# Kernel optimization log

Measured on AMD Instinct MI355X. Metric: run time of the kernel, lower is better.

The kernel has to match this reference:

```python
import jax, jax.numpy as jnp
import numpy as np
import math

# Model dims (from init_kwargs + mamba_ssm Mamba2 defaults)
D_MODEL = 1024
EXPAND = 2
HEADDIM = 64
D_STATE = 64
D_CONV = 4
NGROUPS = 1
D_INNER = EXPAND * D_MODEL            # 2048
NHEADS = D_INNER // HEADDIM           # 32
CONV_DIM = D_INNER + 2 * NGROUPS * D_STATE   # 2176
D_IN_PROJ = 2 * D_INNER + 2 * NGROUPS * D_STATE + NHEADS  # 4256
BATCH, SEQLEN = 4, 2048
RMS_EPS = 1.1920929e-07   # torch.finfo(float32).eps (nn.RMSNorm eps=None)
GNORM_EPS = 1e-5          # mamba_ssm RMSNormGated eps


def _rmsnorm(x, w, eps):
    return x * jax.lax.rsqrt(jnp.mean(x * x, axis=-1, keepdims=True) + eps) * w


def setup_inputs() -> dict:
    key = jax.random.key(0)
    ks = jax.random.split(key, 8)
    x = jax.random.normal(ks[0], (BATCH, SEQLEN, D_MODEL), jnp.float32)
    # router MLP (Linear(d_model,32) -> SiLU -> Linear(32,3))
    r_w1 = jax.random.normal(ks[1], (32, D_MODEL), jnp.float32) / math.sqrt(D_MODEL)
    r_b1 = jnp.zeros((32,), jnp.float32)
    r_w2 = jax.random.normal(ks[2], (3, 32), jnp.float32) / math.sqrt(32)
    r_b2 = jnp.zeros((3,), jnp.float32)
    # Mamba2 params
    in_proj_w = jax.random.normal(ks[3], (D_IN_PROJ, D_MODEL), jnp.float32) / math.sqrt(D_MODEL)
    conv_w = jax.random.normal(ks[4], (CONV_DIM, D_CONV), jnp.float32) * 0.2
    conv_b = jnp.zeros((CONV_DIM,), jnp.float32)
    dt_bias = jax.random.normal(ks[5], (NHEADS,), jnp.float32) * 0.1
    # OrthoSSM multi-scale override: A_log[i] = log(0.001 * 2**i)
    A_log = jnp.log(0.001 * (2.0 ** jnp.arange(NHEADS, dtype=jnp.float32)))
    D_param = jnp.ones((NHEADS,), jnp.float32)
    gnorm_w = jnp.ones((D_INNER,), jnp.float32)
    out_proj_w = jax.random.normal(ks[6], (D_MODEL, D_INNER), jnp.float32) / math.sqrt(D_INNER)
    norm_w = jnp.ones((D_MODEL,), jnp.float32)
    return {"x": x, "norm_w": norm_w, "r_w1": r_w1, "r_b1": r_b1, "r_w2": r_w2,
            "r_b2": r_b2, "in_proj_w": in_proj_w, "conv_w": conv_w, "conv_b": conv_b,
            "dt_bias": dt_bias, "A_log": A_log, "D_param": D_param,
            "gnorm_w": gnorm_w, "out_proj_w": out_proj_w}


def _forward(x, norm_w, r_w1, r_b1, r_w2, r_b2, in_proj_w, conv_w, conv_b,
             dt_bias, A_log, D_param, gnorm_w, out_proj_w):
    B, S, Dm = x.shape
    x_norm = _rmsnorm(x, norm_w, RMS_EPS)
    # --- router: mean-pool -> tiny MLP -> softmax over 3 tiers ---
    h = jax.nn.silu(x_norm.mean(axis=1) @ r_w1.T + r_b1)
    probs = jax.nn.softmax(h @ r_w2.T + r_b2, axis=-1)   # [B,3]
    p_fast = probs[:, 0][:, None, None]
    p_mamba = (probs[:, 1] + probs[:, 2])[:, None, None]
    # --- Mamba2(x_norm) ---
    zxbcdt = x_norm @ in_proj_w.T                         # [B,S,4256]
    z, xBC, dt = jnp.split(zxbcdt, [D_INNER, D_INNER + CONV_DIM], axis=-1)
    # causal depthwise conv1d (kernel 4) + SiLU
    conv = jax.lax.conv_general_dilated(
        xBC.transpose(0, 2, 1), conv_w[:, None, :], (1,), [(D_CONV - 1, 0)],
        feature_group_count=CONV_DIM)                      # [B,CONV_DIM,S]
    xBC = jax.nn.silu(conv.transpose(0, 2, 1) + conv_b)    # [B,S,CONV_DIM]
    xh, Bmat, Cmat = jnp.split(xBC, [D_INNER, D_INNER + NGROUPS * D_STATE], axis=-1)
    xh = xh.reshape(B, S, NHEADS, HEADDIM)                 # [B,S,H,P]
    dt = jax.nn.softplus(dt + dt_bias)                     # [B,S,H]
    A = -jnp.exp(A_log)                                    # [H]
    dA = jnp.exp(dt * A)                                   # [B,S,H]

    def step(hstate, inp):
        dA_t, dt_t, x_t, B_t, C_t = inp
        # hstate: [B,H,P,N]
        hstate = hstate * dA_t[..., None, None] \
                 + (dt_t[..., None] * x_t)[..., None] * B_t[:, None, None, :]
        y_t = jnp.einsum('bhpn,bn->bhp', hstate, C_t)
        return hstate, y_t

    h0 = jnp.zeros((B, NHEADS, HEADDIM, D_STATE), x.dtype)
    xs = (dA.transpose(1, 0, 2), dt.transpose(1, 0, 2), xh.transpose(1, 0, 2, 3),
          Bmat.transpose(1, 0, 2), Cmat.transpose(1, 0, 2))
    _, ys = jax.lax.scan(step, h0, xs)                     # [S,B,H,P]
    y = ys.transpose(1, 0, 2, 3) + D_param[:, None] * xh   # D skip connection
    y = y.reshape(B, S, D_INNER)
    # gated RMSNorm: norm(y * silu(z)) * weight
    yg = y * jax.nn.silu(z)
    yg = _rmsnorm(yg, gnorm_w, GNORM_EPS)
    mamba_out = yg @ out_proj_w.T                          # [B,S,D]
    out = p_fast * x_norm + p_mamba * mamba_out
    return x + out


def reference(x, norm_w, r_w1, r_b1, r_w2, r_b2, in_proj_w, conv_w, conv_b,
              dt_bias, A_log, D_param, gnorm_w, out_proj_w):
    return _forward(x, norm_w, r_w1, r_b1, r_w2, r_b2, in_proj_w, conv_w, conv_b,
                    dt_bias, A_log, D_param, gnorm_w, out_proj_w)
```

## Files before the change

kernel.cpp:

```cpp
#include <hip/hip_runtime.h>
#include <math.h>

typedef __bf16 bf16;
typedef __bf16 bf16x8 __attribute__((ext_vector_type(8)));
typedef __bf16 bf16x4 __attribute__((ext_vector_type(4)));
typedef float f32x4 __attribute__((ext_vector_type(4)));

#define DEV static __device__ __forceinline__
#define AS1 __attribute__((address_space(1)))
#define AS3 __attribute__((address_space(3)))

constexpr int kBatch = 4, kSeq = 2048, kDModel = 1024;
constexpr int kDInner = 2048, kHeads = 32;
constexpr int kConvDim = 2176, kDInProj = 4256, kNPad1 = 4352;
constexpr int kRows = kBatch * kSeq;
constexpr int kChunk = 64, kNChunk = kSeq / kChunk;
constexpr float kRmsEps = 1.1920929e-07f;
constexpr float kGnEps = 1e-5f;
constexpr int kW1Blocks = kNPad1 * kDModel / 256;
constexpr int kW2Blocks = kDModel * kDInner / 1024;

DEV float siluf(float x) { return x / (1.f + expf(-x)); }

DEV float block_reduce_sum(float v, float* red, int tid) {
#pragma unroll
  for (int m = 1; m < 64; m <<= 1) v += __shfl_xor(v, m);
  if ((tid & 63) == 0) red[tid >> 6] = v;
  __syncthreads();
  return red[0] + red[1] + red[2] + red[3];
}

__global__ __launch_bounds__(256) void k_pre(
    const float* __restrict__ x, const float* __restrict__ nw,
    bf16* __restrict__ xnb, float* __restrict__ rs,
    const float* __restrict__ w1, bf16* __restrict__ w1b,
    const float* __restrict__ w2, const float* __restrict__ gw,
    bf16* __restrict__ w2b) {
  const int blk = blockIdx.x;
  const int tid = threadIdx.x;
  if (blk < kRows) {
    const int row = blk;
    float4 v = ((const float4*)(x + (size_t)row * kDModel))[tid];
    __shared__ float red[4];
    float ss = block_reduce_sum(v.x * v.x + v.y * v.y + v.z * v.z + v.w * v.w, red, tid);
    float scale = rsqrtf(ss * (1.f / kDModel) + kRmsEps);
    if (tid == 0) rs[row] = scale;
    float4 wv = ((const float4*)nw)[tid];
    bf16x4 ov;
    ov[0] = (bf16)(v.x * scale * wv.x);
    ov[1] = (bf16)(v.y * scale * wv.y);
    ov[2] = (bf16)(v.z * scale * wv.z);
    ov[3] = (bf16)(v.w * scale * wv.w);
    *(bf16x4*)(xnb + (size_t)row * kDModel + tid * 4) = ov;
  } else if (blk < kRows + kW1Blocks) {
    const size_t idx = (size_t)(blk - kRows) * 256 + tid;
    const int row = (int)(idx >> 10);
    w1b[idx] = (bf16)(row < kDInProj ? w1[idx] : 0.f);
  } else {
    const size_t i4 = (size_t)(blk - kRows - kW1Blocks) * 256 + tid;
    const int k4 = (int)((i4 * 4) & (kDInner - 1));
    float4 v = ((const float4*)w2)[i4];
    float4 g = *(const float4*)(gw + k4);
    bf16x4 o;
    o[0] = (bf16)(v.x * g.x); o[1] = (bf16)(v.y * g.y);
    o[2] = (bf16)(v.z * g.z); o[3] = (bf16)(v.w * g.w);
    ((bf16x4*)w2b)[i4] = o;
  }
}

__global__ __launch_bounds__(128) void k_pool1(const bf16* __restrict__ xnb,
                                               float* __restrict__ part) {
  const int g = blockIdx.x, b = blockIdx.y;
  const int tid = threadIdx.x;
  const bf16* base = xnb + ((size_t)b * kSeq + (size_t)g * 32) * kDModel + tid * 8;
  float acc[8] = {0, 0, 0, 0, 0, 0, 0, 0};
  for (int r = 0; r < 32; ++r) {
    bf16x8 v = *(const bf16x8*)(base + (size_t)r * kDModel);
#pragma unroll
    for (int j = 0; j < 8; ++j) acc[j] += (float)v[j];
  }
  float* o = part + ((size_t)b * 64 + g) * kDModel + tid * 8;
#pragma unroll
  for (int j = 0; j < 8; ++j) o[j] = acc[j];
}

__global__ __launch_bounds__(256) void k_pool2(const float* __restrict__ part,
                                               float* __restrict__ mean) {
  const int idx = blockIdx.x * 256 + threadIdx.x;
  const int b = idx >> 10, d = idx & 1023;
  float s = 0.f;
  for (int g = 0; g < 64; ++g) s += part[((size_t)b * 64 + g) * kDModel + d];
  mean[idx] = s * (1.f / kSeq);
}

__global__ __launch_bounds__(128) void k_router(const float* __restrict__ mean,
                                                const float* __restrict__ w1,
                                                const float* __restrict__ b1,
                                                const float* __restrict__ w2,
                                                const float* __restrict__ b2,
                                                float* __restrict__ pfm) {
  __shared__ float hbuf[4][32];
  __shared__ float logit[4][3];
  const int t = threadIdx.x;
  {
    int b = t >> 5, j = t & 31;
    float s = b1[j];
    for (int d = 0; d < kDModel; ++d) s += mean[b * kDModel + d] * w1[j * kDModel + d];
    hbuf[b][j] = siluf(s);
  }
  __syncthreads();
  if (t < 12) {
    int b = t / 3, k = t % 3;
    float s = b2[k];
    for (int j = 0; j < 32; ++j) s += hbuf[b][j] * w2[k * 32 + j];
    logit[b][k] = s;
  }
  __syncthreads();
  if (t < 4) {
    float m = fmaxf(logit[t][0], fmaxf(logit[t][1], logit[t][2]));
    float e0 = expf(logit[t][0] - m), e1 = expf(logit[t][1] - m), e2 = expf(logit[t][2] - m);
    float inv = 1.f / (e0 + e1 + e2);
    pfm[t] = e0 * inv;
    pfm[4 + t] = (e1 + e2) * inv;
  }
}

template <int WM, int WN, int NF, bool FUSE>
DEV void gemm_body(bf16* lds, float* rs2s,
                   const bf16* __restrict__ A, const bf16* __restrict__ B,
                   bf16* __restrict__ Cb, const float* __restrict__ xres,
                   const float* __restrict__ rs, const float* __restrict__ nw,
                   const float* __restrict__ pfm, float* __restrict__ outf,
                   int K, int Nreal, int ldc, int ntn) {
  constexpr int THREADS = WM * WN * 64;
  constexpr int BM = WM * 64;
  constexpr int BN = WN * NF * 16;
  constexpr int NA = (BM * 4) / THREADS;
  constexpr int NB = (BN * 4) / THREADS;
  constexpr int VMN = NA + NB;
  constexpr int ASZ = (BM / 2) * 64;
  constexpr int BSZ = (BN / 2) * 64;
  const int tid = threadIdx.x;
  const int lane = tid & 63, wid = tid >> 6;
  const int wr = wid / WN, wc = wid % WN;
  const int lr = lane & 15, kb = lane >> 4;
  const int cpx = (int)gridDim.x >> 3;
  const int bid = ((int)blockIdx.x & 7) * cpx + ((int)blockIdx.x >> 3);
  const long n0 = (long)(bid % ntn) * BN;
  const long m0 = (long)(bid / ntn) * BM;

  f32x4 acc[4][NF];
#pragma unroll
  for (int i = 0; i < 4; ++i)
#pragma unroll
    for (int j = 0; j < NF; ++j) acc[i][j] = (f32x4){0.f, 0.f, 0.f, 0.f};
  float ssq[4] = {0.f, 0.f, 0.f, 0.f};

  const int nkt = K >> 5;

#define STAGE(pp, kt)                                                          \
  {                                                                            \
    const long koff = (long)(kt)*32;                                           \
    _Pragma("unroll") for (int j = 0; j < NA; ++j) {                           \
      int idx = j * THREADS + tid;                                             \
      int line = idx >> 3, sp = (idx & 7) ^ (line & 7);                        \
      int row = line * 2 + (sp >> 2), ch = sp & 3;                             \
      __builtin_amdgcn_global_load_lds(                                        \
          (const AS1 void*)(A + (m0 + row) * K + koff + ch * 8),               \
          (AS3 void*)((char*)(lds + (pp)*ASZ) + idx * 16), 16, 0, 0);          \
    }                                                                          \
    _Pragma("unroll") for (int j = 0; j < NB; ++j) {                           \
      int idx = j * THREADS + tid;                                             \
      int line = idx >> 3, sp = (idx & 7) ^ (line & 7);                        \
      int row = line * 2 + (sp >> 2), ch = sp & 3;                             \
      __builtin_amdgcn_global_load_lds(                                        \
          (const AS1 void*)(B + (n0 + row) * K + koff + ch * 8),               \
          (AS3 void*)((char*)(lds + 3 * ASZ + (pp)*BSZ) + idx * 16), 16, 0, 0);\
    }                                                                          \
  }
#define LOFF(r) (((r) >> 1) * 128 + (((((r)&1) << 2) | kb) ^ (((r) >> 1) & 7)) * 16)
#define RDA(pp, r) (*(const bf16x8*)((const char*)(lds + (pp)*ASZ) + LOFF(r)))
#define RDB(pp, r) (*(const bf16x8*)((const char*)(lds + 3 * ASZ + (pp)*BSZ) + LOFF(r)))

  STAGE(0, 0);
  STAGE(1, 1);

  int cur = 0;
  for (int t = 0; t < nkt; ++t) {
    if (t + 2 < nkt) {
      int sb = cur + 2; if (sb >= 3) sb -= 3;
      STAGE(sb, t + 2);
      if constexpr (VMN == 3) asm volatile("s_waitcnt vmcnt(6)" ::: "memory");
      else asm volatile("s_waitcnt vmcnt(8)" ::: "memory");
    } else if (t + 1 < nkt) {
      if constexpr (VMN == 3) asm volatile("s_waitcnt vmcnt(3)" ::: "memory");
      else asm volatile("s_waitcnt vmcnt(4)" ::: "memory");
    } else {
      asm volatile("s_waitcnt vmcnt(0)" ::: "memory");
    }
    __builtin_amdgcn_s_barrier();

    bf16x8 bv[NF], af0, af1, af2, af3;
#pragma unroll
    for (int nf = 0; nf < NF; ++nf) bv[nf] = RDB(cur, wc * (NF * 16) + nf * 16 + lr);
    af0 = RDA(cur, wr * 64 + lr);
    __builtin_amdgcn_sched_barrier(0);
    af1 = RDA(cur, wr * 64 + 16 + lr);
    __builtin_amdgcn_sched_barrier(0);
    asm volatile("s_waitcnt lgkmcnt(1)" ::: "memory");
    __builtin_amdgcn_sched_barrier(0);
    __builtin_amdgcn_s_setprio(1);
#pragma unroll
    for (int nf = 0; nf < NF; ++nf)
      acc[0][nf] = __builtin_amdgcn_mfma_f32_16x16x32_bf16(af0, bv[nf], acc[0][nf], 0, 0, 0);
    af2 = RDA(cur, wr * 64 + 32 + lr);
    af3 = RDA(cur, wr * 64 + 48 + lr);
    __builtin_amdgcn_sched_barrier(0);
    asm volatile("s_waitcnt lgkmcnt(2)" ::: "memory");
    __builtin_amdgcn_sched_barrier(0);
#pragma unroll
    for (int nf = 0; nf < NF; ++nf)
      acc[1][nf] = __builtin_amdgcn_mfma_f32_16x16x32_bf16(af1, bv[nf], acc[1][nf], 0, 0, 0);
    asm volatile("s_waitcnt lgkmcnt(0)" ::: "memory");
    __builtin_amdgcn_sched_barrier(0);
    __builtin_amdgcn_s_barrier();
#pragma unroll
    for (int nf = 0; nf < NF; ++nf)
      acc[2][nf] = __builtin_amdgcn_mfma_f32_16x16x32_bf16(af2, bv[nf], acc[2][nf], 0, 0, 0);
#pragma unroll
    for (int nf = 0; nf < NF; ++nf)
      acc[3][nf] = __builtin_amdgcn_mfma_f32_16x16x32_bf16(af3, bv[nf], acc[3][nf], 0, 0, 0);
    __builtin_amdgcn_s_setprio(0);

    if constexpr (FUSE) {
      if (wc == 0) {
#pragma unroll
        for (int e = 0; e < 8; ++e) {
          float f0 = (float)af0[e], f1 = (float)af1[e];
          float f2 = (float)af2[e], f3 = (float)af3[e];
          ssq[0] = fmaf(f0, f0, ssq[0]);
          ssq[1] = fmaf(f1, f1, ssq[1]);
          ssq[2] = fmaf(f2, f2, ssq[2]);
          ssq[3] = fmaf(f3, f3, ssq[3]);
        }
      }
    }
    cur = cur + 1 == 3 ? 0 : cur + 1;
  }
#undef STAGE
#undef LOFF
#undef RDA
#undef RDB

  const int rr = kb * 4;
  if constexpr (FUSE) {
    if (wc == 0) {
#pragma unroll
      for (int mf = 0; mf < 4; ++mf) {
        float v = ssq[mf];
        v += __shfl_xor(v, 16);
        v += __shfl_xor(v, 32);
        if (kb == 0) rs2s[wr * 64 + mf * 16 + lr] = rsqrtf(v * (1.f / kDInner) + kGnEps);
      }
    }
    __syncthreads();
    const int bx = (int)(m0 >> 11);
    const float pf = pfm[bx], pm = pfm[4 + bx];
#pragma unroll
    for (int mf = 0; mf < 4; ++mf) {
      long rbase = m0 + wr * 64 + mf * 16 + rr;
      float rsv[4], r2v[4];
#pragma unroll
      for (int j = 0; j < 4; ++j) {
        rsv[j] = rs[rbase + j];
        r2v[j] = rs2s[wr * 64 + mf * 16 + rr + j];
      }
#pragma unroll
      for (int nf = 0; nf < NF; ++nf) {
        int col = (int)n0 + wc * (NF * 16) + nf * 16 + lr;
        float wv = nw[col];
#pragma unroll
        for (int j = 0; j < 4; ++j) {
          size_t oi = (size_t)(rbase + j) * kDModel + col;
          float xv = xres[oi];
          outf[oi] = xv + pf * xv * rsv[j] * wv + pm * r2v[j] * acc[mf][nf][j];
        }
      }
    }
  } else {
    __syncthreads();
    bf16* scr = lds + wid * (16 * 72);
    const int srow = lane >> 2, cg = lane & 3;
#pragma unroll
    for (int mf = 0; mf < 4; ++mf) {
#pragma unroll
      for (int nf = 0; nf < NF; ++nf)
#pragma unroll
        for (int j = 0; j < 4; ++j)
          scr[(rr + j) * 72 + nf * 16 + lr] = (bf16)acc[mf][nf][j];
      asm volatile("s_waitcnt lgkmcnt(0)" ::: "memory");
      __builtin_amdgcn_sched_barrier(0);
      int col = (int)n0 + wc * (NF * 16) + cg * 16;
      if (col < Nreal) {
        long grow = m0 + wr * 64 + mf * 16 + srow;
        bf16x8 v0 = *(const bf16x8*)(scr + srow * 72 + cg * 16);
        bf16x8 v1 = *(const bf16x8*)(scr + srow * 72 + cg * 16 + 8);
        *(bf16x8*)(Cb + grow * (long)ldc + col) = v0;
        *(bf16x8*)(Cb + grow * (long)ldc + col + 8) = v1;
      }
      __builtin_amdgcn_sched_barrier(0);
    }
  }
}

__global__ __launch_bounds__(512, 4) void k_gemm_in(
    const bf16* __restrict__ A, const bf16* __restrict__ B,
    bf16* __restrict__ Cb, int K, int Nreal, int ldc, int ntn) {
  constexpr int ASZ = (128 / 2) * 64, BSZ = (256 / 2) * 64;
  __shared__ __align__(16) bf16 lds[3 * ASZ + 3 * BSZ];
  __shared__ float rs2s[128];
  gemm_body<2, 4, 4, false>(lds, rs2s, A, B, Cb, nullptr, nullptr, nullptr,
                            nullptr, nullptr, K, Nreal, ldc, ntn);
}

__global__ __launch_bounds__(256, 4) void k_gemm_out(
    const bf16* __restrict__ A, const bf16* __restrict__ B,
    const float* __restrict__ xres, const float* __restrict__ rs,
    const float* __restrict__ nw, const float* __restrict__ pfm,
    float* __restrict__ outf, int K, int Nreal, int ldc, int ntn) {
  constexpr int ASZ = (64 / 2) * 64, BSZ = (128 / 2) * 64;
  __shared__ __align__(16) bf16 lds[3 * ASZ + 3 * BSZ];
  __shared__ float rs2s[64];
  gemm_body<1, 4, 2, true>(lds, rs2s, A, B, nullptr, xres, rs, nw, pfm, outf,
                           K, Nreal, ldc, ntn);
}

__global__ __launch_bounds__(256) void k_convdt(const bf16* __restrict__ zx,
                                                const float* __restrict__ cw,
                                                const float* __restrict__ cb,
                                                bf16* __restrict__ xbc,
                                                const float* __restrict__ dt_bias,
                                                const float* __restrict__ A_log,
                                                float* __restrict__ dt,
                                                float* __restrict__ ldA) {
  const int gid = blockIdx.x * 256 + threadIdx.x;
  if (gid < kRows * 272) {
    const int row = gid / 272;
    const int cg = gid - row * 272;
    const int c0 = cg * 8;
    const int s = row & (kSeq - 1);
    const bf16* base = zx + (size_t)row * kDInProj + kDInner + c0;
    bf16x8 z8 = {};
    bf16x8 r3 = *(const bf16x8*)(base);
    bf16x8 r2 = (s >= 1) ? *(const bf16x8*)(base - kDInProj) : z8;
    bf16x8 r1 = (s >= 2) ? *(const bf16x8*)(base - 2 * kDInProj) : z8;
    bf16x8 r0 = (s >= 3) ? *(const bf16x8*)(base - 3 * kDInProj) : z8;
    bf16x8 o;
#pragma unroll
    for (int e = 0; e < 8; ++e) {
      float4 w = ((const float4*)cw)[c0 + e];
      float a = cb[c0 + e] + w.x * (float)r0[e] + w.y * (float)r1[e] +
                w.z * (float)r2[e] + w.w * (float)r3[e];
      o[e] = (bf16)siluf(a);
    }
    *(bf16x8*)(xbc + (size_t)row * kConvDim + c0) = o;
  } else {
    const int g2 = gid - kRows * 272;
    const int row = g2 >> 2, grp = g2 & 3;
    bf16x8 r8 = *(const bf16x8*)(zx + (size_t)row * kDInProj + (kDInner + kConvDim) + grp * 8);
#pragma unroll
    for (int e = 0; e < 8; ++e) {
      int hh = grp * 8 + e;
      float raw = (float)r8[e] + dt_bias[hh];
      float dtv = (raw > 20.f) ? raw : log1pf(expf(raw));
      dt[row * kHeads + hh] = dtv;
      ldA[row * kHeads + hh] = dtv * -expf(A_log[hh]);
    }
  }
}

__global__ __launch_bounds__(256) void k_chunkA(
    const bf16* __restrict__ xbc, const float* __restrict__ dtb,
    const float* __restrict__ ldab, float* __restrict__ cumbuf,
    float* __restrict__ Tc, bf16* __restrict__ yb, bf16* __restrict__ Sbuf) {
  const int c = blockIdx.x, h = blockIdx.y, b = blockIdx.z;
  const int tid = threadIdx.x;
  const int w = tid >> 6, lane = tid & 63, lr = lane & 15, kb = lane >> 4;
  const int rr = kb * 4;
  const int t0 = c * kChunk;
  __shared__ bf16 Bl[64 * 72], Cl[64 * 72], XT[64 * 72], WBT[64 * 72], Ml[64 * 72];
  __shared__ float cum_s[64], dt_s[64], w_s[64];

  {
    int s = tid >> 2, q = tid & 3;
    const bf16* rowp = xbc + ((size_t)b * kSeq + t0 + s) * kConvDim;
    bf16x8 x0 = *(const bf16x8*)(rowp + h * 64 + q * 16);
    bf16x8 x1 = *(const bf16x8*)(rowp + h * 64 + q * 16 + 8);
    bf16x8 b0 = *(const bf16x8*)(rowp + kDInner + q * 16);
    bf16x8 b1 = *(const bf16x8*)(rowp + kDInner + q * 16 + 8);
    bf16x8 c0 = *(const bf16x8*)(rowp + kDInner + 64 + q * 16);
    bf16x8 c1 = *(const bf16x8*)(rowp + kDInner + 64 + q * 16 + 8);
    *(bf16x8*)(Bl + s * 72 + q * 16) = b0;
    *(bf16x8*)(Bl + s * 72 + q * 16 + 8) = b1;
    *(bf16x8*)(Cl + s * 72 + q * 16) = c0;
    *(bf16x8*)(Cl + s * 72 + q * 16 + 8) = c1;
#pragma unroll
    for (int e = 0; e < 8; ++e) XT[(q * 16 + e) * 72 + s] = x0[e];
#pragma unroll
    for (int e = 0; e < 8; ++e) XT[(q * 16 + 8 + e) * 72 + s] = x1[e];
  }
  if (tid < 64) {
    size_t di = ((size_t)b * kSeq + t0 + tid) * kHeads + h;
    float v = ldab[di];
    float dtv = dtb[di];
#pragma unroll
    for (int o = 1; o < 64; o <<= 1) {
      float u = __shfl_up(v, o);
      if (lane >= o) v += u;
    }
    cum_s[tid] = v;
    dt_s[tid] = dtv;
    float tot = __shfl(v, 63);
    w_s[tid] = expf(tot - v) * dtv;
    cumbuf[(((size_t)b * kHeads + h) * kNChunk + c) * 64 + tid] = v;
    if (tid == 63) Tc[(b * kHeads + h) * kNChunk + c] = expf(v);
  }
  __syncthreads();

#pragma unroll
  for (int i = 0; i < 16; ++i) {
    int e = i * 256 + tid;
    int n = e >> 6, s = e & 63;
    WBT[n * 72 + s] = (bf16)((float)Bl[s * 72 + n] * w_s[s]);
  }

  f32x4 g[4];
#pragma unroll
  for (int nt = 0; nt < 4; ++nt) g[nt] = (f32x4){0.f, 0.f, 0.f, 0.f};
#pragma unroll
  for (int kk = 0; kk < 2; ++kk) {
    bf16x8 a = *(const bf16x8*)(Cl + (w * 16 + lr) * 72 + kk * 32 + kb * 8);
#pragma unroll
    for (int nt = 0; nt < 4; ++nt) {
      bf16x8 bb = *(const bf16x8*)(Bl + (nt * 16 + lr) * 72 + kk * 32 + kb * 8);
      g[nt] = __builtin_amdgcn_mfma_f32_16x16x32_bf16(a, bb, g[nt], 0, 0, 0);
    }
  }
#pragma unroll
  for (int nt = 0; nt < 4; ++nt)
#pragma unroll
    for (int j = 0; j < 4; ++j) {
      int tt = w * 16 + rr + j, ss = nt * 16 + lr;
      float m = (ss <= tt) ? g[nt][j] * expf(cum_s[tt] - cum_s[ss]) * dt_s[ss] : 0.f;
      Ml[tt * 72 + ss] = (bf16)m;
    }
  __syncthreads();

  f32x4 y4[4];
#pragma unroll
  for (int pt = 0; pt < 4; ++pt) y4[pt] = (f32x4){0.f, 0.f, 0.f, 0.f};
#pragma unroll
  for (int kk = 0; kk < 2; ++kk) {
    bf16x8 a = *(const bf16x8*)(Ml + (w * 16 + lr) * 72 + kk * 32 + kb * 8);
#pragma unroll
    for (int pt = 0; pt < 4; ++pt) {
      bf16x8 bb = *(const bf16x8*)(XT + (pt * 16 + lr) * 72 + kk * 32 + kb * 8);
      y4[pt] = __builtin_amdgcn_mfma_f32_16x16x32_bf16(a, bb, y4[pt], 0, 0, 0);
    }
  }
  f32x4 s4[4];
#pragma unroll
  for (int nt = 0; nt < 4; ++nt) s4[nt] = (f32x4){0.f, 0.f, 0.f, 0.f};
#pragma unroll
  for (int kk = 0; kk < 2; ++kk) {
    bf16x8 a = *(const bf16x8*)(XT + (w * 16 + lr) * 72 + kk * 32 + kb * 8);
#pragma unroll
    for (int nt = 0; nt < 4; ++nt) {
      bf16x8 bb = *(const bf16x8*)(WBT + (nt * 16 + lr) * 72 + kk * 32 + kb * 8);
      s4[nt] = __builtin_amdgcn_mfma_f32_16x16x32_bf16(a, bb, s4[nt], 0, 0, 0);
    }
  }
#pragma unroll
  for (int pt = 0; pt < 4; ++pt)
#pragma unroll
    for (int j = 0; j < 4; ++j) {
      Bl[(w * 16 + rr + j) * 72 + pt * 16 + lr] = (bf16)y4[pt][j];
      Cl[(w * 16 + rr + j) * 72 + pt * 16 + lr] = (bf16)s4[pt][j];
    }
  __syncthreads();
  {
    int row = tid >> 2, cg = tid & 3;
    bf16x8 v0 = *(const bf16x8*)(Bl + row * 72 + cg * 16);
    bf16x8 v1 = *(const bf16x8*)(Bl + row * 72 + cg * 16 + 8);
    bf16* dst = yb + ((size_t)b * kSeq + t0 + row) * kDInner + h * 64 + cg * 16;
    *(bf16x8*)dst = v0;
    *(bf16x8*)(dst + 8) = v1;
    const size_t sbase = (((size_t)b * kHeads + h) * kNChunk + c) * 4096;
    bf16x8 u0 = *(const bf16x8*)(Cl + row * 72 + cg * 16);
    bf16x8 u1 = *(const bf16x8*)(Cl + row * 72 + cg * 16 + 8);
    bf16* sdst = Sbuf + sbase + row * 64 + cg * 16;
    *(bf16x8*)sdst = u0;
    *(bf16x8*)(sdst + 8) = u1;
  }
}

__global__ __launch_bounds__(256) void k_chunkB(bf16* __restrict__ S,
                                                const float* __restrict__ Tc) {
  const int gid = blockIdx.x * 256 + threadIdx.x;
  const int bh = gid >> 10;
  const int pn = (gid & 1023) << 2;
  bf16* base = S + (size_t)bh * kNChunk * 4096 + pn;
  const float* tc = Tc + bh * kNChunk;
  float4 hh = {0.f, 0.f, 0.f, 0.f};
  bf16x4 s = *(const bf16x4*)(base);
  for (int c = 0; c < kNChunk; ++c) {
    bf16x4 sn = {};
    if (c + 1 < kNChunk) sn = *(const bf16x4*)(base + (size_t)(c + 1) * 4096);
    float t = tc[c];
    bf16x4 ho;
    ho[0] = (bf16)hh.x; ho[1] = (bf16)hh.y; ho[2] = (bf16)hh.z; ho[3] = (bf16)hh.w;
    *(bf16x4*)(base + (size_t)c * 4096) = ho;
    hh.x = t * hh.x + (float)s[0];
    hh.y = t * hh.y + (float)s[1];
    hh.z = t * hh.z + (float)s[2];
    hh.w = t * hh.w + (float)s[3];
    s = sn;
  }
}

__global__ __launch_bounds__(256) void k_chunkC(
    const bf16* __restrict__ xbc, const bf16* __restrict__ zx,
    const float* __restrict__ cumbuf, const bf16* __restrict__ hs,
    const float* __restrict__ Dp, bf16* __restrict__ yb) {
  const int c = blockIdx.x, h = blockIdx.y, b = blockIdx.z;
  const int tid = threadIdx.x;
  const int w = tid >> 6, lane = tid & 63, lr = lane & 15, kb = lane >> 4;
  const int rr = kb * 4;
  const int t0 = c * kChunk;
  __shared__ bf16 Cl[64 * 72];
  __shared__ float ecum[64];
  __shared__ float scrf[64 * 68];
  {
    int s = tid >> 2, q = tid & 3;
    const bf16* rowp = xbc + ((size_t)b * kSeq + t0 + s) * kConvDim + kDInner + 64 + q * 16;
    *(bf16x8*)(Cl + s * 72 + q * 16) = *(const bf16x8*)rowp;
    *(bf16x8*)(Cl + s * 72 + q * 16 + 8) = *(const bf16x8*)(rowp + 8);
  }
  if (tid < 64)
    ecum[tid] = expf(cumbuf[(((size_t)b * kHeads + h) * kNChunk + c) * 64 + tid]);
  __syncthreads();

  const bf16* hbase = hs + (((size_t)b * kHeads + h) * kNChunk + c) * 4096;
  f32x4 acc[4];
#pragma unroll
  for (int pt = 0; pt < 4; ++pt) acc[pt] = (f32x4){0.f, 0.f, 0.f, 0.f};
#pragma unroll
  for (int kk = 0; kk < 2; ++kk) {
    bf16x8 a = *(const bf16x8*)(Cl + (w * 16 + lr) * 72 + kk * 32 + kb * 8);
#pragma unroll
    for (int pt = 0; pt < 4; ++pt) {
      bf16x8 bb = *(const bf16x8*)(hbase + (pt * 16 + lr) * 64 + kk * 32 + kb * 8);
      acc[pt] = __builtin_amdgcn_mfma_f32_16x16x32_bf16(a, bb, acc[pt], 0, 0, 0);
    }
  }
#pragma unroll
  for (int pt = 0; pt < 4; ++pt)
#pragma unroll
    for (int j = 0; j < 4; ++j) {
      int tt = w * 16 + rr + j;
      scrf[tt * 68 + pt * 16 + lr] = ecum[tt] * acc[pt][j];
    }
  __syncthreads();
  {
    const float Dh = Dp[h];
    int row = tid >> 2, cg = tid & 3;
    size_t ri = (size_t)b * kSeq + t0 + row;
    const float* sp = scrf + row * 68 + cg * 16;
    bf16* yp = yb + ri * kDInner + h * 64 + cg * 16;
    const bf16* xp = xbc + ri * kConvDim + h * 64 + cg * 16;
    const bf16* zp = zx + ri * kDInProj + h * 64 + cg * 16;
#pragma unroll
    for (int half = 0; half < 2; ++half) {
      bf16x8 yv = *(const bf16x8*)(yp + half * 8);
      bf16x8 xv = *(const bf16x8*)(xp + half * 8);
      bf16x8 zv = *(const bf16x8*)(zp + half * 8);
      bf16x8 o;
#pragma unroll
      for (int e = 0; e < 8; ++e) {
        float yfull = (float)yv[e] + sp[half * 8 + e] + Dh * (float)xv[e];
        o[e] = (bf16)(yfull * siluf((float)zv[e]));
      }
      *(bf16x8*)(yp + half * 8) = o;
    }
  }
}

extern "C" void kernel_launch(void* const* d_in, const int* in_sizes, int n_in,
                              void* d_out, int out_size, void* d_ws, size_t ws_size,
                              hipStream_t stream) {
  const float* x = (const float*)d_in[0];
  const float* norm_w = (const float*)d_in[1];
  const float* r_w1 = (const float*)d_in[2];
  const float* r_b1 = (const float*)d_in[3];
  const float* r_w2 = (const float*)d_in[4];
  const float* r_b2 = (const float*)d_in[5];
  const float* in_proj_w = (const float*)d_in[6];
  const float* conv_w = (const float*)d_in[7];
  const float* conv_b = (const float*)d_in[8];
  const float* dt_bias = (const float*)d_in[9];
  const float* A_log = (const float*)d_in[10];
  const float* D_param = (const float*)d_in[11];
  const float* gnorm_w = (const float*)d_in[12];
  const float* out_proj_w = (const float*)d_in[13];
  float* out = (float*)d_out;
  char* ws = (char*)d_ws;

  bf16* xnb     = (bf16*)(ws + 0);
  bf16* w1b     = (bf16*)(ws + 16777216);
  bf16* zx      = (bf16*)(ws + 25690112);
  bf16* xbc     = (bf16*)(ws + 95420416);
  float* dtb    = (float*)(ws + 131072000);
  float* ldab   = (float*)(ws + 132120576);
  float* cumbuf = (float*)(ws + 133169152);
  float* Tcb    = (float*)(ws + 134217728);
  bf16* yb      = (bf16*)(ws + 134234112);
  bf16* Sbuf    = (bf16*)(ws + 167788544);
  bf16* w2b     = (bf16*)(ws + 201342976);
  float* part   = (float*)(ws + 205537280);
  float* meanb  = (float*)(ws + 206585856);
  float* pfm    = (float*)(ws + 206602240);
  float* rsb    = (float*)(ws + 206602368);

  k_pre<<<kRows + kW1Blocks + kW2Blocks, 256, 0, stream>>>(
      x, norm_w, xnb, rsb, in_proj_w, w1b, out_proj_w, gnorm_w, w2b);
  k_pool1<<<dim3(64, 4), 128, 0, stream>>>(xnb, part);
  k_pool2<<<16, 256, 0, stream>>>(part, meanb);
  k_router<<<1, 128, 0, stream>>>(meanb, r_w1, r_b1, r_w2, r_b2, pfm);
  k_gemm_in<<<(kRows / 128) * (kNPad1 / 256), 512, 0, stream>>>(
      xnb, w1b, zx, kDModel, kDInProj, kDInProj, kNPad1 / 256);
  k_convdt<<<(kRows * 272 + kRows * 4) / 256, 256, 0, stream>>>(
      zx, conv_w, conv_b, xbc, dt_bias, A_log, dtb, ldab);
  k_chunkA<<<dim3(kNChunk, kHeads, kBatch), 256, 0, stream>>>(
      xbc, dtb, ldab, cumbuf, Tcb, yb, Sbuf);
  k_chunkB<<<512, 256, 0, stream>>>(Sbuf, Tcb);
  k_chunkC<<<dim3(kNChunk, kHeads, kBatch), 256, 0, stream>>>(
      xbc, zx, cumbuf, Sbuf, D_param, yb);
  k_gemm_out<<<(kRows / 64) * (kDModel / 128), 256, 0, stream>>>(
      yb, w2b, x, rsb, norm_w, pfm, out,
      kDInner, kDModel, kDModel, kDModel / 128);
}
```

Baseline: 344.6 us.

## Rewrite in_proj GEMM with 256x256 tiles and phased double-buffered LDS pipeline

Replaces the generic in_proj GEMM with a dedicated 256x256-tile kernel that uses XOR-swizzled, direct-to-LDS loads. The LDS buffers are double-buffered, and each k-tile is split into sub-phases that overlap staging of the next tiles with MFMA work. Each block also gets an XCD-aware remapping of block ids. The larger tile raises arithmetic intensity and data reuse, at the cost of more registers and LDS (occupancy 2) and half as many blocks. The shared GEMM body used by the output projection is also simplified: all A fragments load up front and the MFMA issue is a single loop, dropping the earlier interleaving of loads and MFMAs.

```diff
diff --git a/kernel.cpp b/kernel.cpp
--- a/kernel.cpp
+++ b/kernel.cpp
@@ -125,6 +125,128 @@
   }
 }
 
+__global__ __launch_bounds__(512, 2) void k_gemm_in(
+    const bf16* __restrict__ A, const bf16* __restrict__ B,
+    bf16* __restrict__ Cb, int K, int Nreal, int ldc, int ntn) {
+  __shared__ __align__(16) bf16 Al[2][2][128 * 64];
+  __shared__ __align__(16) bf16 Bl[2][2][128 * 64];
+  const int tid = threadIdx.x;
+  const int lane = tid & 63, wid = tid >> 6;
+  const int wr = wid >> 2, wc = wid & 3;
+  const int lr = lane & 15, kb = lane >> 4;
+  const int cpx = (int)gridDim.x >> 3;
+  const int bid = ((int)blockIdx.x & 7) * cpx + ((int)blockIdx.x >> 3);
+  const long n0 = (long)(bid % ntn) * 256;
+  const long m0 = (long)(bid / ntn) * 256;
+
+  f32x4 acc[8][4];
+#pragma unroll
+  for (int i = 0; i < 8; ++i)
+#pragma unroll
+    for (int j = 0; j < 4; ++j) acc[i][j] = (f32x4){0.f, 0.f, 0.f, 0.f};
+
+  const int ntile = K >> 6;
+  const int niter = K >> 7;
+
+#define STG(P, dst, rowbase, kt)                                               \
+  { _Pragma("unroll") for (int j = 0; j < 2; ++j) {                            \
+      int idx = j * 512 + tid;                                                 \
+      int line = idx >> 3, ch = (idx & 7) ^ (line & 7);                        \
+      __builtin_amdgcn_global_load_lds(                                        \
+          (const AS1 void*)((P) + ((rowbase) + line) * (long)K +               \
+                            (long)(kt)*64 + ch * 8),                           \
+          (AS3 void*)((char*)(dst) + idx * 16), 16, 0, 0);                     \
+  } }
+#define RD(bufptr, r, c)                                                       \
+  (*(const bf16x8*)((const char*)(bufptr) + (r)*128 + (((c) ^ ((r)&7)) * 16)))
+
+  STG(A, Al[0][0], m0, 0);
+  STG(A, Al[0][1], m0 + 128, 0);
+  STG(B, Bl[0][0], n0, 0);
+  STG(B, Bl[0][1], n0 + 128, 0);
+  STG(B, Bl[1][0], n0, 1);
+  STG(B, Bl[1][1], n0 + 128, 1);
+  asm volatile("s_waitcnt vmcnt(4)" ::: "memory");
+  __builtin_amdgcn_s_barrier();
+
+  bf16x8 bfr[4][2];
+
+#define PHASE(PAR, PP, RDB_FLAG, STAGE_STMT, VM_STMT)                          \
+  {                                                                            \
+    if (RDB_FLAG) {                                                            \
+      _Pragma("unroll") for (int nf = 0; nf < 4; ++nf) {                       \
+        bfr[nf][0] = RD(Bl[PAR][wc >> 1], (wc & 1) * 64 + nf * 16 + lr, kb);   \
+        bfr[nf][1] = RD(Bl[PAR][wc >> 1], (wc & 1) * 64 + nf * 16 + lr, 4 + kb); \
+      }                                                                        \
+    }                                                                          \
+    bf16x8 af00 = RD(Al[PAR][wr], (2 * (PP)) * 16 + lr, kb);                   \
+    bf16x8 af01 = RD(Al[PAR][wr], (2 * (PP)) * 16 + lr, 4 + kb);               \
+    bf16x8 af10 = RD(Al[PAR][wr], (2 * (PP) + 1) * 16 + lr, kb);               \
+    bf16x8 af11 = RD(Al[PAR][wr], (2 * (PP) + 1) * 16 + lr, 4 + kb);           \
+    STAGE_STMT;                                                                \
+    VM_STMT;                                                                   \
+    __builtin_amdgcn_s_barrier();                                              \
+    asm volatile("s_waitcnt lgkmcnt(0)" ::: "memory");                         \
+    __builtin_amdgcn_sched_barrier(0);                                         \
+    __builtin_amdgcn_s_setprio(1);                                             \
+    _Pragma("unroll") for (int nf = 0; nf < 4; ++nf) {                         \
+      acc[2 * (PP)][nf] = __builtin_amdgcn_mfma_f32_16x16x32_bf16(             \
+          af00, bfr[nf][0], acc[2 * (PP)][nf], 0, 0, 0);                       \
+      acc[2 * (PP)][nf] = __builtin_amdgcn_mfma_f32_16x16x32_bf16(             \
+          af01, bfr[nf][1], acc[2 * (PP)][nf], 0, 0, 0);                       \
+      acc[2 * (PP) + 1][nf] = __builtin_amdgcn_mfma_f32_16x16x32_bf16(         \
+          af10, bfr[nf][0], acc[2 * (PP) + 1][nf], 0, 0, 0);                   \
+      acc[2 * (PP) + 1][nf] = __builtin_amdgcn_mfma_f32_16x16x32_bf16(         \
+          af11, bfr[nf][1], acc[2 * (PP) + 1][nf], 0, 0, 0);                   \
+    }                                                                          \
+    __builtin_amdgcn_s_setprio(0);                                             \
+    __builtin_amdgcn_s_barrier();                                              \
+  }
+
+  for (int i = 0; i < niter; ++i) {
+    const int t1 = 2 * i + 1, t2 = 2 * i + 2, t3 = 2 * i + 3;
+    const bool g2 = t2 < ntile, g3 = t3 < ntile;
+    PHASE(0, 0, 1, STG(A, Al[1][0], m0, t1), );
+    PHASE(0, 1, 0, STG(A, Al[1][1], m0 + 128, t1), );
+    PHASE(0, 2, 0, if (g2) STG(B, Bl[0][0], n0, t2), );
+    PHASE(0, 3, 0, if (g2) STG(B, Bl[0][1], n0 + 128, t2),
+          if (g2) { asm volatile("s_waitcnt vmcnt(4)" ::: "memory"); }
+          else { asm volatile("s_waitcnt vmcnt(0)" ::: "memory"); });
+    PHASE(1, 0, 1, if (g2) STG(A, Al[0][0], m0, t2), );
+    PHASE(1, 1, 0, if (g2) STG(A, Al[0][1], m0 + 128, t2), );
+    PHASE(1, 2, 0, if (g3) STG(B, Bl[1][0], n0, t3), );
+    PHASE(1, 3, 0, if (g3) STG(B, Bl[1][1], n0 + 128, t3),
+          if (g3) { asm volatile("s_waitcnt vmcnt(4)" ::: "memory"); });
+  }
+#undef PHASE
+#undef STG
+#undef RD
+
+  __syncthreads();
+  bf16* scr = &Al[0][0][0] + wid * (16 * 72);
+  const int rr = kb * 4;
+  const int srow = lane >> 2, cg = lane & 3;
+#pragma unroll
+  for (int mf = 0; mf < 8; ++mf) {
+#pragma unroll
+    for (int nf = 0; nf < 4; ++nf)
+#pragma unroll
+      for (int j = 0; j < 4; ++j)
+        scr[(rr + j) * 72 + nf * 16 + lr] = (bf16)acc[mf][nf][j];
+    asm volatile("s_waitcnt lgkmcnt(0)" ::: "memory");
+    __builtin_amdgcn_sched_barrier(0);
+    int col = (int)n0 + wc * 64 + cg * 16;
+    if (col < Nreal) {
+      long grow = m0 + wr * 128 + mf * 16 + srow;
+      bf16x8 v0 = *(const bf16x8*)(scr + srow * 72 + cg * 16);
+      bf16x8 v1 = *(const bf16x8*)(scr + srow * 72 + cg * 16 + 8);
+      *(bf16x8*)(Cb + grow * (long)ldc + col) = v0;
+      *(bf16x8*)(Cb + grow * (long)ldc + col + 8) = v1;
+    }
+    __builtin_amdgcn_sched_barrier(0);
+  }
+}
+
 template <int WM, int WN, int NF, bool FUSE>
 DEV void gemm_body(bf16* lds, float* rs2s,
                    const bf16* __restrict__ A, const bf16* __restrict__ B,
@@ -200,51 +322,34 @@
     }
     __builtin_amdgcn_s_barrier();
 
-    bf16x8 bv[NF], af0, af1, af2, af3;
+    bf16x8 af[4], bv[NF];
+#pragma unroll
+    for (int mf = 0; mf < 4; ++mf) af[mf] = RDA(cur, wr * 64 + mf * 16 + lr);
 #pragma unroll
     for (int nf = 0; nf < NF; ++nf) bv[nf] = RDB(cur, wc * (NF * 16) + nf * 16 + lr);
-    af0 = RDA(cur, wr * 64 + lr);
-    __builtin_amdgcn_sched_barrier(0);
-    af1 = RDA(cur, wr * 64 + 16 + lr);
-    __builtin_amdgcn_sched_barrier(0);
-    asm volatile("s_waitcnt lgkmcnt(1)" ::: "memory");
-    __builtin_amdgcn_sched_barrier(0);
-    __builtin_amdgcn_s_setprio(1);
-#pragma unroll
-    for (int nf = 0; nf < NF; ++nf)
-      acc[0][nf] = __builtin_amdgcn_mfma_f32_16x16x32_bf16(af0, bv[nf], acc[0][nf], 0, 0, 0);
-    af2 = RDA(cur, wr * 64 + 32 + lr);
-    af3 = RDA(cur, wr * 64 + 48 + lr);
-    __builtin_amdgcn_sched_barrier(0);
-    asm volatile("s_waitcnt lgkmcnt(2)" ::: "memory");
-    __builtin_amdgcn_sched_barrier(0);
-#pragma unroll
-    for (int nf = 0; nf < NF; ++nf)
-      acc[1][nf] = __builtin_amdgcn_mfma_f32_16x16x32_bf16(af1, bv[nf], acc[1][nf], 0, 0, 0);
     asm volatile("s_waitcnt lgkmcnt(0)" ::: "memory");
     __builtin_amdgcn_sched_barrier(0);
     __builtin_amdgcn_s_barrier();
-#pragma unroll
-    for (int nf = 0; nf < NF; ++nf)
-      acc[2][nf] = __builtin_amdgcn_mfma_f32_16x16x32_bf16(af2, bv[nf], acc[2][nf], 0, 0, 0);
-#pragma unroll
-    for (int nf = 0; nf < NF; ++nf)
-      acc[3][nf] = __builtin_amdgcn_mfma_f32_16x16x32_bf16(af3, bv[nf], acc[3][nf], 0, 0, 0);
-    __builtin_amdgcn_s_setprio(0);
 
     if constexpr (FUSE) {
       if (wc == 0) {
 #pragma unroll
-        for (int e = 0; e < 8; ++e) {
-          float f0 = (float)af0[e], f1 = (float)af1[e];
-          float f2 = (float)af2[e], f3 = (float)af3[e];
-          ssq[0] = fmaf(f0, f0, ssq[0]);
-          ssq[1] = fmaf(f1, f1, ssq[1]);
-          ssq[2] = fmaf(f2, f2, ssq[2]);
-          ssq[3] = fmaf(f3, f3, ssq[3]);
-        }
+        for (int mf = 0; mf < 4; ++mf)
+#pragma unroll
+          for (int e = 0; e < 8; ++e) {
+            float f = (float)af[mf][e];
+            ssq[mf] = fmaf(f, f, ssq[mf]);
+          }
       }
     }
+    __builtin_amdgcn_s_setprio(1);
+#pragma unroll
+    for (int mf = 0; mf < 4; ++mf)
+#pragma unroll
+      for (int nf = 0; nf < NF; ++nf)
+        acc[mf][nf] = __builtin_amdgcn_mfma_f32_16x16x32_bf16(af[mf], bv[nf],
+                                                              acc[mf][nf], 0, 0, 0);
+    __builtin_amdgcn_s_setprio(0);
     cur = cur + 1 == 3 ? 0 : cur + 1;
   }
 #undef STAGE
@@ -311,16 +416,6 @@
       __builtin_amdgcn_sched_barrier(0);
     }
   }
-}
-
-__global__ __launch_bounds__(512, 4) void k_gemm_in(
-    const bf16* __restrict__ A, const bf16* __restrict__ B,
-    bf16* __restrict__ Cb, int K, int Nreal, int ldc, int ntn) {
-  constexpr int ASZ = (128 / 2) * 64, BSZ = (256 / 2) * 64;
-  __shared__ __align__(16) bf16 lds[3 * ASZ + 3 * BSZ];
-  __shared__ float rs2s[128];
-  gemm_body<2, 4, 4, false>(lds, rs2s, A, B, Cb, nullptr, nullptr, nullptr,
-                            nullptr, nullptr, K, Nreal, ldc, ntn);
 }
 
 __global__ __launch_bounds__(256, 4) void k_gemm_out(
@@ -636,7 +731,7 @@
   k_pool1<<<dim3(64, 4), 128, 0, stream>>>(xnb, part);
   k_pool2<<<16, 256, 0, stream>>>(part, meanb);
   k_router<<<1, 128, 0, stream>>>(meanb, r_w1, r_b1, r_w2, r_b2, pfm);
-  k_gemm_in<<<(kRows / 128) * (kNPad1 / 256), 512, 0, stream>>>(
+  k_gemm_in<<<(kRows / 256) * (kNPad1 / 256), 512, 0, stream>>>(
       xnb, w1b, zx, kDModel, kDInProj, kDInProj, kNPad1 / 256);
   k_convdt<<<(kRows * 272 + kRows * 4) / 256, 256, 0, stream>>>(
       zx, conv_w, conv_b, xbc, dt_bias, A_log, dtb, ldab);
```

Result: slower. 356.0 us (+3.3%).

## Move intra-chunk diagonal output computation from chunkA into chunkC

Applied to the files above, without the earlier changes.

The intra-chunk diagonal term (C·Bᵀ masked and decayed, times X) moves from the chunk-state kernel into the final output kernel. There it is summed in registers with the inter-chunk state contribution, so the bf16 partial y is no longer written to global memory and read back. This removes one bf16 round trip of y through global memory and one rounding step. In exchange chunkC must reload B and X and uses more shared memory, which may lower occupancy, while chunkA becomes lighter.

```diff
diff --git a/kernel.cpp b/kernel.cpp
--- a/kernel.cpp
+++ b/kernel.cpp
@@ -382,14 +382,14 @@
 __global__ __launch_bounds__(256) void k_chunkA(
     const bf16* __restrict__ xbc, const float* __restrict__ dtb,
     const float* __restrict__ ldab, float* __restrict__ cumbuf,
-    float* __restrict__ Tc, bf16* __restrict__ yb, bf16* __restrict__ Sbuf) {
+    float* __restrict__ Tc, bf16* __restrict__ Sbuf) {
   const int c = blockIdx.x, h = blockIdx.y, b = blockIdx.z;
   const int tid = threadIdx.x;
   const int w = tid >> 6, lane = tid & 63, lr = lane & 15, kb = lane >> 4;
   const int rr = kb * 4;
   const int t0 = c * kChunk;
-  __shared__ bf16 Bl[64 * 72], Cl[64 * 72], XT[64 * 72], WBT[64 * 72], Ml[64 * 72];
-  __shared__ float cum_s[64], dt_s[64], w_s[64];
+  __shared__ bf16 Bl[64 * 72], XT[64 * 72], WBT[64 * 72];
+  __shared__ float w_s[64];
 
   {
     int s = tid >> 2, q = tid & 3;
@@ -398,12 +398,8 @@
     bf16x8 x1 = *(const bf16x8*)(rowp + h * 64 + q * 16 + 8);
     bf16x8 b0 = *(const bf16x8*)(rowp + kDInner + q * 16);
     bf16x8 b1 = *(const bf16x8*)(rowp + kDInner + q * 16 + 8);
-    bf16x8 c0 = *(const bf16x8*)(rowp + kDInner + 64 + q * 16);
-    bf16x8 c1 = *(const bf16x8*)(rowp + kDInner + 64 + q * 16 + 8);
     *(bf16x8*)(Bl + s * 72 + q * 16) = b0;
     *(bf16x8*)(Bl + s * 72 + q * 16 + 8) = b1;
-    *(bf16x8*)(Cl + s * 72 + q * 16) = c0;
-    *(bf16x8*)(Cl + s * 72 + q * 16 + 8) = c1;
 #pragma unroll
     for (int e = 0; e < 8; ++e) XT[(q * 16 + e) * 72 + s] = x0[e];
 #pragma unroll
@@ -418,8 +414,6 @@
       float u = __shfl_up(v, o);
       if (lane >= o) v += u;
     }
-    cum_s[tid] = v;
-    dt_s[tid] = dtv;
     float tot = __shfl(v, 63);
     w_s[tid] = expf(tot - v) * dtv;
     cumbuf[(((size_t)b * kHeads + h) * kNChunk + c) * 64 + tid] = v;
@@ -433,41 +427,8 @@
     int n = e >> 6, s = e & 63;
     WBT[n * 72 + s] = (bf16)((float)Bl[s * 72 + n] * w_s[s]);
   }
-
-  f32x4 g[4];
-#pragma unroll
-  for (int nt = 0; nt < 4; ++nt) g[nt] = (f32x4){0.f, 0.f, 0.f, 0.f};
-#pragma unroll
-  for (int kk = 0; kk < 2; ++kk) {
-    bf16x8 a = *(const bf16x8*)(Cl + (w * 16 + lr) * 72 + kk * 32 + kb * 8);
-#pragma unroll
-    for (int nt = 0; nt < 4; ++nt) {
-      bf16x8 bb = *(const bf16x8*)(Bl + (nt * 16 + lr) * 72 + kk * 32 + kb * 8);
-      g[nt] = __builtin_amdgcn_mfma_f32_16x16x32_bf16(a, bb, g[nt], 0, 0, 0);
-    }
-  }
-#pragma unroll
-  for (int nt = 0; nt < 4; ++nt)
-#pragma unroll
-    for (int j = 0; j < 4; ++j) {
-      int tt = w * 16 + rr + j, ss = nt * 16 + lr;
-      float m = (ss <= tt) ? g[nt][j] * expf(cum_s[tt] - cum_s[ss]) * dt_s[ss] : 0.f;
-      Ml[tt * 72 + ss] = (bf16)m;
-    }
-  __syncthreads();
-
-  f32x4 y4[4];
-#pragma unroll
-  for (int pt = 0; pt < 4; ++pt) y4[pt] = (f32x4){0.f, 0.f, 0.f, 0.f};
-#pragma unroll
-  for (int kk = 0; kk < 2; ++kk) {
-    bf16x8 a = *(const bf16x8*)(Ml + (w * 16 + lr) * 72 + kk * 32 + kb * 8);
-#pragma unroll
-    for (int pt = 0; pt < 4; ++pt) {
-      bf16x8 bb = *(const bf16x8*)(XT + (pt * 16 + lr) * 72 + kk * 32 + kb * 8);
-      y4[pt] = __builtin_amdgcn_mfma_f32_16x16x32_bf16(a, bb, y4[pt], 0, 0, 0);
-    }
-  }
+  __syncthreads();
+
   f32x4 s4[4];
 #pragma unroll
   for (int nt = 0; nt < 4; ++nt) s4[nt] = (f32x4){0.f, 0.f, 0.f, 0.f};
@@ -481,23 +442,16 @@
     }
   }
 #pragma unroll
-  for (int pt = 0; pt < 4; ++pt)
-#pragma unroll
-    for (int j = 0; j < 4; ++j) {
-      Bl[(w * 16 + rr + j) * 72 + pt * 16 + lr] = (bf16)y4[pt][j];
-      Cl[(w * 16 + rr + j) * 72 + pt * 16 + lr] = (bf16)s4[pt][j];
-    }
+  for (int nt = 0; nt < 4; ++nt)
+#pragma unroll
+    for (int j = 0; j < 4; ++j)
+      Bl[(w * 16 + rr + j) * 72 + nt * 16 + lr] = (bf16)s4[nt][j];
   __syncthreads();
   {
     int row = tid >> 2, cg = tid & 3;
-    bf16x8 v0 = *(const bf16x8*)(Bl + row * 72 + cg * 16);
-    bf16x8 v1 = *(const bf16x8*)(Bl + row * 72 + cg * 16 + 8);
-    bf16* dst = yb + ((size_t)b * kSeq + t0 + row) * kDInner + h * 64 + cg * 16;
-    *(bf16x8*)dst = v0;
-    *(bf16x8*)(dst + 8) = v1;
     const size_t sbase = (((size_t)b * kHeads + h) * kNChunk + c) * 4096;
-    bf16x8 u0 = *(const bf16x8*)(Cl + row * 72 + cg * 16);
-    bf16x8 u1 = *(const bf16x8*)(Cl + row * 72 + cg * 16 + 8);
+    bf16x8 u0 = *(const bf16x8*)(Bl + row * 72 + cg * 16);
+    bf16x8 u1 = *(const bf16x8*)(Bl + row * 72 + cg * 16 + 8);
     bf16* sdst = Sbuf + sbase + row * 64 + cg * 16;
     *(bf16x8*)sdst = u0;
     *(bf16x8*)(sdst + 8) = u1;
@@ -530,37 +484,90 @@
 
 __global__ __launch_bounds__(256) void k_chunkC(
     const bf16* __restrict__ xbc, const bf16* __restrict__ zx,
-    const float* __restrict__ cumbuf, const bf16* __restrict__ hs,
-    const float* __restrict__ Dp, bf16* __restrict__ yb) {
+    const float* __restrict__ dtb, const float* __restrict__ cumbuf,
+    const bf16* __restrict__ hs, const float* __restrict__ Dp,
+    bf16* __restrict__ yb) {
   const int c = blockIdx.x, h = blockIdx.y, b = blockIdx.z;
   const int tid = threadIdx.x;
   const int w = tid >> 6, lane = tid & 63, lr = lane & 15, kb = lane >> 4;
   const int rr = kb * 4;
   const int t0 = c * kChunk;
-  __shared__ bf16 Cl[64 * 72];
-  __shared__ float ecum[64];
+  __shared__ bf16 Bl[64 * 72], Cl[64 * 72], XT[64 * 72], Ml[64 * 72];
+  __shared__ float cum_s[64], dt_s[64], ecum[64];
   __shared__ float scrf[64 * 68];
+
   {
     int s = tid >> 2, q = tid & 3;
-    const bf16* rowp = xbc + ((size_t)b * kSeq + t0 + s) * kConvDim + kDInner + 64 + q * 16;
-    *(bf16x8*)(Cl + s * 72 + q * 16) = *(const bf16x8*)rowp;
-    *(bf16x8*)(Cl + s * 72 + q * 16 + 8) = *(const bf16x8*)(rowp + 8);
-  }
-  if (tid < 64)
-    ecum[tid] = expf(cumbuf[(((size_t)b * kHeads + h) * kNChunk + c) * 64 + tid]);
-  __syncthreads();
-
-  const bf16* hbase = hs + (((size_t)b * kHeads + h) * kNChunk + c) * 4096;
-  f32x4 acc[4];
-#pragma unroll
-  for (int pt = 0; pt < 4; ++pt) acc[pt] = (f32x4){0.f, 0.f, 0.f, 0.f};
+    const bf16* rowp = xbc + ((size_t)b * kSeq + t0 + s) * kConvDim;
+    bf16x8 x0 = *(const bf16x8*)(rowp + h * 64 + q * 16);
+    bf16x8 x1 = *(const bf16x8*)(rowp + h * 64 + q * 16 + 8);
+    bf16x8 b0 = *(const bf16x8*)(rowp + kDInner + q * 16);
+    bf16x8 b1 = *(const bf16x8*)(rowp + kDInner + q * 16 + 8);
+    bf16x8 c0 = *(const bf16x8*)(rowp + kDInner + 64 + q * 16);
+    bf16x8 c1 = *(const bf16x8*)(rowp + kDInner + 64 + q * 16 + 8);
+    *(bf16x8*)(Bl + s * 72 + q * 16) = b0;
+    *(bf16x8*)(Bl + s * 72 + q * 16 + 8) = b1;
+    *(bf16x8*)(Cl + s * 72 + q * 16) = c0;
+    *(bf16x8*)(Cl + s * 72 + q * 16 + 8) = c1;
+#pragma unroll
+    for (int e = 0; e < 8; ++e) XT[(q * 16 + e) * 72 + s] = x0[e];
+#pragma unroll
+    for (int e = 0; e < 8; ++e) XT[(q * 16 + 8 + e) * 72 + s] = x1[e];
+  }
+  if (tid < 64) {
+    size_t di = ((size_t)b * kSeq + t0 + tid) * kHeads + h;
+    float cv = cumbuf[(((size_t)b * kHeads + h) * kNChunk + c) * 64 + tid];
+    cum_s[tid] = cv;
+    ecum[tid] = expf(cv);
+    dt_s[tid] = dtb[di];
+  }
+  __syncthreads();
+
+  f32x4 g[4];
+#pragma unroll
+  for (int nt = 0; nt < 4; ++nt) g[nt] = (f32x4){0.f, 0.f, 0.f, 0.f};
 #pragma unroll
   for (int kk = 0; kk < 2; ++kk) {
     bf16x8 a = *(const bf16x8*)(Cl + (w * 16 + lr) * 72 + kk * 32 + kb * 8);
 #pragma unroll
+    for (int nt = 0; nt < 4; ++nt) {
+      bf16x8 bb = *(const bf16x8*)(Bl + (nt * 16 + lr) * 72 + kk * 32 + kb * 8);
+      g[nt] = __builtin_amdgcn_mfma_f32_16x16x32_bf16(a, bb, g[nt], 0, 0, 0);
+    }
+  }
+#pragma unroll
+  for (int nt = 0; nt < 4; ++nt)
+#pragma unroll
+    for (int j = 0; j < 4; ++j) {
+      int tt = w * 16 + rr + j, ss = nt * 16 + lr;
+      float m = (ss <= tt) ? g[nt][j] * expf(cum_s[tt] - cum_s[ss]) * dt_s[ss] : 0.f;
+      Ml[tt * 72 + ss] = (bf16)m;
+    }
+  __syncthreads();
+
+  f32x4 y4[4];
+#pragma unroll
+  for (int pt = 0; pt < 4; ++pt) y4[pt] = (f32x4){0.f, 0.f, 0.f, 0.f};
+#pragma unroll
+  for (int kk = 0; kk < 2; ++kk) {
+    bf16x8 a = *(const bf16x8*)(Ml + (w * 16 + lr) * 72 + kk * 32 + kb * 8);
+#pragma unroll
+    for (int pt = 0; pt < 4; ++pt) {
+      bf16x8 bb = *(const bf16x8*)(XT + (pt * 16 + lr) * 72 + kk * 32 + kb * 8);
+      y4[pt] = __builtin_amdgcn_mfma_f32_16x16x32_bf16(a, bb, y4[pt], 0, 0, 0);
+    }
+  }
+  const bf16* hbase = hs + (((size_t)b * kHeads + h) * kNChunk + c) * 4096;
+  f32x4 acc2[4];
+#pragma unroll
+  for (int pt = 0; pt < 4; ++pt) acc2[pt] = (f32x4){0.f, 0.f, 0.f, 0.f};
+#pragma unroll
+  for (int kk = 0; kk < 2; ++kk) {
+    bf16x8 a = *(const bf16x8*)(Cl + (w * 16 + lr) * 72 + kk * 32 + kb * 8);
+#pragma unroll
     for (int pt = 0; pt < 4; ++pt) {
       bf16x8 bb = *(const bf16x8*)(hbase + (pt * 16 + lr) * 64 + kk * 32 + kb * 8);
-      acc[pt] = __builtin_amdgcn_mfma_f32_16x16x32_bf16(a, bb, acc[pt], 0, 0, 0);
+      acc2[pt] = __builtin_amdgcn_mfma_f32_16x16x32_bf16(a, bb, acc2[pt], 0, 0, 0);
     }
   }
 #pragma unroll
@@ -568,7 +575,7 @@
 #pragma unroll
     for (int j = 0; j < 4; ++j) {
       int tt = w * 16 + rr + j;
-      scrf[tt * 68 + pt * 16 + lr] = ecum[tt] * acc[pt][j];
+      scrf[tt * 68 + pt * 16 + lr] = y4[pt][j] + ecum[tt] * acc2[pt][j];
     }
   __syncthreads();
   {
@@ -581,13 +588,12 @@
     const bf16* zp = zx + ri * kDInProj + h * 64 + cg * 16;
 #pragma unroll
     for (int half = 0; half < 2; ++half) {
-      bf16x8 yv = *(const bf16x8*)(yp + half * 8);
       bf16x8 xv = *(const bf16x8*)(xp + half * 8);
       bf16x8 zv = *(const bf16x8*)(zp + half * 8);
       bf16x8 o;
 #pragma unroll
       for (int e = 0; e < 8; ++e) {
-        float yfull = (float)yv[e] + sp[half * 8 + e] + Dh * (float)xv[e];
+        float yfull = sp[half * 8 + e] + Dh * (float)xv[e];
         o[e] = (bf16)(yfull * siluf((float)zv[e]));
       }
       *(bf16x8*)(yp + half * 8) = o;
@@ -641,10 +647,10 @@
   k_convdt<<<(kRows * 272 + kRows * 4) / 256, 256, 0, stream>>>(
       zx, conv_w, conv_b, xbc, dt_bias, A_log, dtb, ldab);
   k_chunkA<<<dim3(kNChunk, kHeads, kBatch), 256, 0, stream>>>(
-      xbc, dtb, ldab, cumbuf, Tcb, yb, Sbuf);
+      xbc, dtb, ldab, cumbuf, Tcb, Sbuf);
   k_chunkB<<<512, 256, 0, stream>>>(Sbuf, Tcb);
   k_chunkC<<<dim3(kNChunk, kHeads, kBatch), 256, 0, stream>>>(
-      xbc, zx, cumbuf, Sbuf, D_param, yb);
+      xbc, zx, dtb, cumbuf, Sbuf, D_param, yb);
   k_gemm_out<<<(kRows / 64) * (kDModel / 128), 256, 0, stream>>>(
       yb, w2b, x, rsb, norm_w, pfm, out,
       kDInner, kDModel, kDModel, kDModel / 128);
```

Measured after the change: 343.5 us, median of 2. About the same (-0.3%).
